# Kernel tuning notes

Hardware: AMD Instinct MI355X
Metric: run time of the kernel (lower is better)

Reference implementation:

```python
import jax, jax.numpy as jnp
import numpy as np

NBUS = 33
B33 = [(1,2),(2,3),(3,4),(4,5),(5,6),(6,7),(7,8),(8,9),(9,10),(10,11),(11,12),(12,13),(13,14),(14,15),(15,16),(16,17),(17,18),(2,19),(19,20),(20,21),(21,22),(3,23),(23,24),(24,25),(6,26),(26,27),(27,28),(28,29),(29,30),(30,31),(31,32),(32,33)]


def setup_inputs() -> dict:
    key = jax.random.key(0)
    k1, k2, k3 = jax.random.split(key, 3)
    B, W, M, F = 32, 128, 100, 8
    N, H, GH, K = NBUS, 256, 128, 3
    rng = np.random.default_rng(0)
    br = np.array(B33) - 1
    src = np.concatenate([br[:, 0], br[:, 1]])
    dst = np.concatenate([br[:, 1], br[:, 0]])
    w_half = rng.uniform(0.5, 2.0, size=br.shape[0]).astype(np.float32)
    p = lambda *s: jnp.asarray(rng.normal(0.0, 0.02, size=s).astype(np.float32))
    z = lambda *s: jnp.zeros(s, jnp.float32)
    return {
        'r_seq': jax.random.normal(k1, (B, W, M), jnp.float32),
        'feat_seq': jax.random.normal(k2, (B, W, F), jnp.float32),
        'x_wls_seq': jax.random.normal(k3, (B, W, 2 * N), jnp.float32),
        'edge_index': jnp.asarray(np.stack([src, dst]).astype(np.int32)),
        'edge_weight': jnp.asarray(np.concatenate([w_half, w_half])),
        'pre_w': p(F + 2, GH), 'pre_b': z(GH),
        'tag_w1': p(K + 1, GH, GH), 'tag_b1': z(GH),
        'tag_w2': p(K + 1, GH, GH), 'tag_b2': z(GH),
        'post_w': p(GH, H), 'post_b': z(H),
        'tp_w1': p(M + 2 * N, H), 'tp_b1': z(H),
        'tp_w2': p(H, H), 'tp_b2': z(H),
        'gru_wih0': p(H, 3 * H), 'gru_whh0': p(H, 3 * H), 'gru_bih0': z(3 * H), 'gru_bhh0': z(3 * H),
        'gru_wih1': p(H, 3 * H), 'gru_whh1': p(H, 3 * H), 'gru_bih1': z(3 * H), 'gru_bhh1': z(3 * H),
        'fg_w': p(H, H), 'fg_b': z(H),
        'fs_w': p(H, H), 'fs_b': z(H),
        'gate_w': p(2 * H, H), 'gate_b': z(H),
        'd1_w': p(H, H), 'd1_b': z(H),
        'd2_w': p(H, 2), 'd2_b': z(2),
    }


def _gru_layer(x, wih, whh, bih, bhh):
    # x: (B, W, Din); torch GRU gate order [r, z, n]
    def step(h, xt):
        gi = xt @ wih + bih
        gh = h @ whh + bhh
        ir, iz, inn = jnp.split(gi, 3, axis=-1)
        hr, hz, hn = jnp.split(gh, 3, axis=-1)
        r = jax.nn.sigmoid(ir + hr)
        zt = jax.nn.sigmoid(iz + hz)
        n = jnp.tanh(inn + r * hn)
        h = (1.0 - zt) * n + zt * h
        return h, h
    h0 = jnp.zeros((x.shape[0], whh.shape[0]), x.dtype)
    _, ys = jax.lax.scan(step, h0, jnp.swapaxes(x, 0, 1))
    return jnp.swapaxes(ys, 0, 1)


def _forward(r_seq, feat_seq, x_wls_seq, edge_index, edge_weight,
             pre_w, pre_b, tag_w1, tag_b1, tag_w2, tag_b2, post_w, post_b,
             tp_w1, tp_b1, tp_w2, tp_b2,
             gru_wih0, gru_whh0, gru_bih0, gru_bhh0,
             gru_wih1, gru_whh1, gru_bih1, gru_bhh1,
             fg_w, fg_b, fs_w, fs_b, gate_w, gate_b,
             d1_w, d1_b, d2_w, d2_b):
    B, W, M = r_seq.shape
    N = NBUS
    # ---- spatial branch (batched TAGConv, K=3, 2 layers) ----
    va = x_wls_seq[..., :N, None]
    vm = x_wls_seq[..., N:, None]
    x_nodes = jnp.concatenate([va, vm], axis=-1)                 # (B,W,N,2)
    feat_n = jnp.broadcast_to(feat_seq[:, :, None, :], (B, W, N, feat_seq.shape[-1]))
    gin = jnp.concatenate([feat_n, x_nodes], axis=-1) @ pre_w + pre_b  # (B,W,N,GH)
    g = gin.reshape(B * W, N, gin.shape[-1])
    src, dst = edge_index[0], edge_index[1]
    # gcn_norm (no self-loops), shared across all B*W graph copies
    deg = jnp.zeros((N,), g.dtype).at[dst].add(edge_weight)
    dinv = jnp.where(deg > 0, deg ** -0.5, 0.0)
    norm = dinv[src] * edge_weight * dinv[dst]                   # (E,)

    def prop(h):  # out[i] = sum_{j->i} norm * h[j], batched over graphs
        return jnp.zeros_like(h).at[:, dst].add(h[:, src] * norm[None, :, None])

    def tag(h, Wk, b):  # TAGConv: sum_k A^k h @ W_k + b
        out = h @ Wk[0]
        hk = h
        for k in range(1, Wk.shape[0]):
            hk = prop(hk)
            out = out + hk @ Wk[k]
        return out + b

    g = jax.nn.relu(tag(g, tag_w1, tag_b1))
    g = tag(g, tag_w2, tag_b2)
    g = g.reshape(B, W, N, -1) @ post_w + post_b                 # (B,W,N,H)
    # ---- temporal branch (MLP -> 2-layer GRU); E_time=None skips MHA ----
    s = jnp.concatenate([r_seq, x_wls_seq], axis=-1)
    s = jax.nn.relu(s @ tp_w1 + tp_b1)
    s = jax.nn.relu(s @ tp_w2 + tp_b2)
    s = _gru_layer(s, gru_wih0, gru_whh0, gru_bih0, gru_bhh0)
    s = _gru_layer(s, gru_wih1, gru_whh1, gru_bih1, gru_bhh1)    # (B,W,H)
    # ---- gated fusion + decoder ----
    g_t = g @ fg_w + fg_b                                        # (B,W,N,H)
    s_t = (s @ fs_w + fs_b)[:, :, None, :]                       # (B,W,1,H)
    s_full = jnp.broadcast_to(s_t, g_t.shape)
    alpha = jax.nn.sigmoid(jnp.concatenate([g_t, s_full], axis=-1) @ gate_w + gate_b)
    u = alpha * g_t + (1.0 - alpha) * s_full
    u = jax.nn.relu(u @ d1_w + d1_b) @ d2_w + d2_b               # (B,W,N,2)
    dx = jnp.concatenate([u[..., 0], u[..., 1]], axis=-1)        # (B,W,2N)
    return x_wls_seq + dx


def reference(r_seq, feat_seq, x_wls_seq, edge_index, edge_weight,
              pre_w, pre_b, tag_w1, tag_b1, tag_w2, tag_b2, post_w, post_b,
              tp_w1, tp_b1, tp_w2, tp_b2,
              gru_wih0, gru_whh0, gru_bih0, gru_bhh0,
              gru_wih1, gru_whh1, gru_bih1, gru_bhh1,
              fg_w, fg_b, fs_w, fs_b, gate_w, gate_b,
              d1_w, d1_b, d2_w, d2_b):
    return _forward(r_seq, feat_seq, x_wls_seq, edge_index, edge_weight,
                    pre_w, pre_b, tag_w1, tag_b1, tag_w2, tag_b2, post_w, post_b,
                    tp_w1, tp_b1, tp_w2, tp_b2,
                    gru_wih0, gru_whh0, gru_bih0, gru_bhh0,
                    gru_wih1, gru_whh1, gru_bih1, gru_bhh1,
                    fg_w, fg_b, fs_w, fs_b, gate_w, gate_b,
                    d1_w, d1_b, d2_w, d2_b)
```

## Files before the change

kernel.cpp:

```cpp
#include <hip/hip_runtime.h>
#include <hip/hip_fp16.h>
#include <cmath>

#define DEV __device__ __forceinline__

typedef unsigned short ushortT;
typedef short bs8 __attribute__((ext_vector_type(8)));
typedef float f32x4 __attribute__((ext_vector_type(4)));
typedef _Float16 f16x2 __attribute__((ext_vector_type(2)));

constexpr int kBW = 4096;
constexpr int kM = 100, kF = 8, kN = 33, kH = 256, kGH = 128, kE = 64;

constexpr int OFF_ROWPTR  = 0;
constexpr int OFF_COLSRC  = 64;
constexpr int OFF_COLNORM = 128;
constexpr int OFF_C       = 192;
constexpr int OFF_WC      = 512;
constexpr int OFF_SPRE    = 33280;
constexpr int OFF_GI      = OFF_SPRE + kBW * kH;
constexpr int OFF_SFUSE   = OFF_GI + kBW * 3 * kH;
constexpr int OFF_SGATE   = OFF_SFUSE + kBW * kH;
constexpr int OFF_WQ0     = OFF_SFUSE;
constexpr int OFF_WQ1     = OFF_SFUSE + 98304;
constexpr int WB_TW1  = 0;
constexpr int WB_TW2  = 65536;
constexpr int WB_WC   = 131072;
constexpr int WB_GATE = 163840;
constexpr int WB_D1   = 229376;
constexpr int WB_TOT  = 294912;

DEV float frcp(float x) { return __builtin_amdgcn_rcpf(x); }
DEV float fsig(float x) { return frcp(1.0f + __expf(-x)); }
DEV float ftanh(float x) { float e = __expf(2.0f * x); return 1.0f - 2.0f * frcp(e + 1.0f); }

DEV ushortT f2bf(float x) {
  unsigned u = __float_as_uint(x);
  unsigned r = u + 0x7fffu + ((u >> 16) & 1u);
  return (ushortT)(r >> 16);
}
DEV float bf2f(ushortT u) { return __uint_as_float(((unsigned)u) << 16); }

DEV f32x4 mfma16(bs8 a, bs8 b, f32x4 c) {
  return __builtin_amdgcn_mfma_f32_16x16x32_bf16(a, b, c, 0, 0, 0);
}
DEV bs8 ldb(const ushortT* p) { return *reinterpret_cast<const bs8*>(p); }

#if __has_builtin(__builtin_amdgcn_fdot2)
DEV float dot2(unsigned w, unsigned hp, float acc) {
  f16x2 wv = __builtin_bit_cast(f16x2, w);
  f16x2 hv = __builtin_bit_cast(f16x2, hp);
  return __builtin_amdgcn_fdot2(wv, hv, acc, false);
}
#else
DEV float dot2(unsigned w, unsigned hp, float acc) {
  f16x2 wv = __builtin_bit_cast(f16x2, w);
  f16x2 hv = __builtin_bit_cast(f16x2, hp);
  acc = fmaf((float)wv.x, (float)hv.x, acc);
  acc = fmaf((float)wv.y, (float)hv.y, acc);
  return acc;
}
#endif

__global__ void k_prep(const int* __restrict__ ei, const float* __restrict__ ew,
                       float* __restrict__ ws) {
  if (blockIdx.x != 0 || threadIdx.x != 0) return;
  int* rowptr = (int*)(ws + OFF_ROWPTR);
  int* colsrc = (int*)(ws + OFF_COLSRC);
  float* colnorm = ws + OFF_COLNORM;
  const int* src = ei;
  const int* dst = ei + kE;
  float deg[kN]; int cnt[kN];
  for (int n = 0; n < kN; ++n) { deg[n] = 0.f; cnt[n] = 0; }
  for (int e = 0; e < kE; ++e) { deg[dst[e]] += ew[e]; cnt[dst[e]]++; }
  float dinv[kN];
  for (int n = 0; n < kN; ++n) dinv[n] = deg[n] > 0.f ? 1.0f / sqrtf(deg[n]) : 0.f;
  int pos[kN];
  int run = 0;
  for (int n = 0; n < kN; ++n) { rowptr[n] = run; pos[n] = run; run += cnt[n]; }
  rowptr[kN] = run;
  for (int e = 0; e < kE; ++e) {
    int d = dst[e];
    int p = pos[d]++;
    colsrc[p] = src[e];
    colnorm[p] = dinv[src[e]] * ew[e] * dinv[d];
  }
}

__global__ void k_wcfold(const float* __restrict__ post_w, const float* __restrict__ post_b,
                         const float* __restrict__ fg_w, const float* __restrict__ fg_b,
                         float* __restrict__ ws) {
  const int j = threadIdx.x;
  if ((int)blockIdx.x < kGH) {
    const int k = blockIdx.x;
    float a = 0.f;
    #pragma unroll 4
    for (int m = 0; m < kH; ++m) a = fmaf(post_w[k * kH + m], fg_w[m * kH + j], a);
    ws[OFF_WC + k * kH + j] = a;
  } else {
    float a = fg_b[j];
    #pragma unroll 4
    for (int m = 0; m < kH; ++m) a = fmaf(post_b[m], fg_w[m * kH + j], a);
    ws[OFF_C + j] = a;
  }
}

__global__ void k_wq(const float* __restrict__ w0, const float* __restrict__ w1,
                     float* __restrict__ ws) {
  const int idx = blockIdx.x * 256 + threadIdx.x;
  if (idx >= 2 * 98304) return;
  const int layer = idx / 98304;
  const int rem = idx - layer * 98304;
  const int p = rem / 768, j = rem - p * 768;
  const float* w = layer ? w1 : w0;
  unsigned* dst = (unsigned*)(ws + (layer ? OFF_WQ1 : OFF_WQ0));
  __half2 v = __floats2half2_rn(w[(2 * p) * 768 + j], w[(2 * p + 1) * 768 + j]);
  dst[rem] = *reinterpret_cast<unsigned*>(&v);
}

__global__ void k_wprep(const float* __restrict__ tw1, const float* __restrict__ tw2,
                        const float* __restrict__ gatew, const float* __restrict__ d1w,
                        float* __restrict__ ws) {
  const int idx = blockIdx.x * 256 + threadIdx.x;
  if (idx >= WB_TOT) return;
  ushortT* WB = (ushortT*)(ws + OFF_GI);
  float v; int dst;
  if (idx < 65536) {
    int s = idx >> 14, r = idx & 16383, k = r >> 7, col = r & 127;
    v = tw1[(s << 14) + (k << 7) + col]; dst = WB_TW1 + (s << 14) + (col << 7) + k;
  } else if (idx < 131072) {
    int i = idx - 65536; int s = i >> 14, r = i & 16383, k = r >> 7, col = r & 127;
    v = tw2[(s << 14) + (k << 7) + col]; dst = WB_TW2 + (s << 14) + (col << 7) + k;
  } else if (idx < 163840) {
    int i = idx - 131072; int k = i & 127, col = i >> 7;
    v = ws[OFF_WC + (k << 8) + col]; dst = WB_WC + (col << 7) + k;
  } else if (idx < 229376) {
    int i = idx - 163840; int k = i & 255, col = i >> 8;
    v = gatew[(k << 8) + col]; dst = WB_GATE + (col << 8) + k;
  } else {
    int i = idx - 229376; int k = i & 255, col = i >> 8;
    v = d1w[(k << 8) + col]; dst = WB_D1 + (col << 8) + k;
  }
  WB[dst] = f2bf(v);
}

__global__ __launch_bounds__(256) void k_tpmlp(
    const float* __restrict__ r_seq, const float* __restrict__ x_wls,
    const float* __restrict__ w1, const float* __restrict__ b1,
    const float* __restrict__ w2, const float* __restrict__ b2,
    float* __restrict__ sout) {
  __shared__ float inr[16][kM + 2 * kN];
  __shared__ float h1[16][kH];
  const int bw0 = blockIdx.x * 16, tid = threadIdx.x;
  #pragma unroll
  for (int r = 0; r < 16; ++r) {
    for (int c = tid; c < kM + 2 * kN; c += 256)
      inr[r][c] = (c < kM) ? r_seq[(bw0 + r) * kM + c]
                           : x_wls[(bw0 + r) * 2 * kN + (c - kM)];
  }
  __syncthreads();
  float acc[16];
  {
    const float bb = b1[tid];
    #pragma unroll
    for (int r = 0; r < 16; ++r) acc[r] = bb;
  }
  for (int k = 0; k < kM + 2 * kN; ++k) {
    const float w = w1[k * kH + tid];
    #pragma unroll
    for (int r = 0; r < 16; ++r) acc[r] = fmaf(inr[r][k], w, acc[r]);
  }
  #pragma unroll
  for (int r = 0; r < 16; ++r) h1[r][tid] = fmaxf(acc[r], 0.f);
  __syncthreads();
  {
    const float bb = b2[tid];
    #pragma unroll
    for (int r = 0; r < 16; ++r) acc[r] = bb;
  }
  #pragma unroll 2
  for (int k = 0; k < kH; ++k) {
    const float w = w2[k * kH + tid];
    #pragma unroll
    for (int r = 0; r < 16; ++r) acc[r] = fmaf(h1[r][k], w, acc[r]);
  }
  #pragma unroll
  for (int r = 0; r < 16; ++r) sout[(bw0 + r) * kH + tid] = fmaxf(acc[r], 0.f);
}

__global__ __launch_bounds__(768) void k_gigemm(
    const float* __restrict__ sin, const float* __restrict__ wih,
    const float* __restrict__ bih, float* __restrict__ gi) {
  __shared__ float sr[16][kH];
  const int bw0 = blockIdx.x * 16, tid = threadIdx.x;
  for (int i = tid; i < 16 * kH; i += 768) sr[i >> 8][i & 255] = sin[bw0 * kH + i];
  __syncthreads();
  float acc[16];
  {
    const float bb = bih[tid];
    #pragma unroll
    for (int r = 0; r < 16; ++r) acc[r] = bb;
  }
  #pragma unroll 2
  for (int k = 0; k < kH; ++k) {
    const float w = wih[k * 768 + tid];
    #pragma unroll
    for (int r = 0; r < 16; ++r) acc[r] = fmaf(sr[r][k], w, acc[r]);
  }
  #pragma unroll
  for (int r = 0; r < 16; ++r) gi[(bw0 + r) * 768 + tid] = acc[r];
}

__global__ __launch_bounds__(768, 3) void k_scan(
    const float* __restrict__ gi, const float* __restrict__ wq,
    const float* __restrict__ bhh, float* __restrict__ sout) {
  __shared__ float h[kH];
  __shared__ __align__(16) unsigned hpk[kH / 2];
  __shared__ float gh[3 * kH];
  const int b = blockIdx.x, tid = threadIdx.x;
  const unsigned* wqp = (const unsigned*)wq;
  unsigned wr[128];
  #pragma unroll
  for (int p = 0; p < 128; ++p) wr[p] = wqp[p * 768 + tid];
  if (tid < kH) h[tid] = 0.f;
  if (tid < kH / 2) hpk[tid] = 0u;
  __syncthreads();
  const float bb = bhh[tid];
  for (int t = 0; t < 128; ++t) {
    const float* girow = gi + (b * 128 + t) * 768;
    float a0 = bb, a1 = 0.f, a2 = 0.f, a3 = 0.f;
    #pragma unroll
    for (int q = 0; q < 32; ++q) {
      const uint4 hp = *reinterpret_cast<const uint4*>(hpk + 4 * q);
      a0 = dot2(wr[4 * q + 0], hp.x, a0);
      a1 = dot2(wr[4 * q + 1], hp.y, a1);
      a2 = dot2(wr[4 * q + 2], hp.z, a2);
      a3 = dot2(wr[4 * q + 3], hp.w, a3);
    }
    gh[tid] = (a0 + a1) + (a2 + a3);
    __syncthreads();
    if (tid < kH) {
      float r = fsig(girow[tid] + gh[tid]);
      float z = fsig(girow[kH + tid] + gh[kH + tid]);
      float n = ftanh(fmaf(r, gh[2 * kH + tid], girow[2 * kH + tid]));
      float hn = (1.f - z) * n + z * h[tid];
      h[tid] = hn;
      reinterpret_cast<__half*>(hpk)[tid] = __float2half(hn);
      sout[(b * 128 + t) * kH + tid] = hn;
    }
    __syncthreads();
  }
}

__global__ __launch_bounds__(256) void k_fsgate(
    const float* __restrict__ s1, const float* __restrict__ fsw,
    const float* __restrict__ fsb, const float* __restrict__ gw,
    const float* __restrict__ gb, float* __restrict__ sfuse,
    float* __restrict__ sgate) {
  __shared__ float sr[16][kH], sf[16][kH];
  const int bw0 = blockIdx.x * 16, tid = threadIdx.x;
  for (int i = tid; i < 16 * kH; i += 256) sr[i >> 8][i & 255] = s1[bw0 * kH + i];
  __syncthreads();
  float acc[16];
  {
    const float bb = fsb[tid];
    #pragma unroll
    for (int r = 0; r < 16; ++r) acc[r] = bb;
  }
  #pragma unroll 2
  for (int k = 0; k < kH; ++k) {
    const float w = fsw[k * kH + tid];
    #pragma unroll
    for (int r = 0; r < 16; ++r) acc[r] = fmaf(sr[r][k], w, acc[r]);
  }
  #pragma unroll
  for (int r = 0; r < 16; ++r) { sf[r][tid] = acc[r]; sfuse[(bw0 + r) * kH + tid] = acc[r]; }
  __syncthreads();
  {
    const float bb = gb[tid];
    #pragma unroll
    for (int r = 0; r < 16; ++r) acc[r] = bb;
  }
  #pragma unroll 2
  for (int k = 0; k < kH; ++k) {
    const float w = gw[(kH + k) * kH + tid];
    #pragma unroll
    for (int r = 0; r < 16; ++r) acc[r] = fmaf(sf[r][k], w, acc[r]);
  }
  #pragma unroll
  for (int r = 0; r < 16; ++r) sgate[(bw0 + r) * kH + tid] = acc[r];
}


constexpr int SB0 = 0;
constexpr int SB1 = 36 * 136;
constexpr int S_TOT = 2 * 36 * 136;

DEV void propb(ushortT* __restrict__ dst, const ushortT* __restrict__ src,
               const int* __restrict__ rp, const int* __restrict__ cs,
               const float* __restrict__ cn) {
  for (int idx = threadIdx.x; idx < kN * 64; idx += 512) {
    const int n = idx >> 6, j2 = idx & 63;
    float a0 = 0.f, a1 = 0.f;
    const int p1 = rp[n + 1];
    for (int p = rp[n]; p < p1; ++p) {
      const unsigned v = *(const unsigned*)(src + cs[p] * 136 + 2 * j2);
      const float w = cn[p];
      a0 = fmaf(__uint_as_float(v << 16), w, a0);
      a1 = fmaf(__uint_as_float(v & 0xffff0000u), w, a1);
    }
    *(unsigned*)(dst + n * 136 + 2 * j2) = (unsigned)f2bf(a0) | ((unsigned)f2bf(a1) << 16);
  }
}

template <bool RELU>
DEV void tag_mfma(ushortT* __restrict__ Sb, const ushortT* __restrict__ WT,
                  const float* __restrict__ b, const int* __restrict__ rp,
                  const int* __restrict__ cs, const float* __restrict__ cn,
                  int wv, int lane) {
  const int lr = lane & 15, lg = lane >> 4;
  const int col = wv * 16 + lr;
  f32x4 acc[3];
  #pragma unroll
  for (int i = 0; i < 3; ++i) acc[i] = (f32x4){0.f, 0.f, 0.f, 0.f};
  #pragma unroll
  for (int s = 0; s < 4; ++s) {
    const ushortT* A = Sb + ((s & 1) ? SB1 : SB0);
    ushortT* Bn      = Sb + ((s & 1) ? SB0 : SB1);
    #pragma unroll
    for (int ks = 0; ks < 4; ++ks) {
      const int kof = ks * 32 + lg * 8;
      bs8 a0 = ldb(A + (lr) * 136 + kof);
      bs8 a1 = ldb(A + (16 + lr) * 136 + kof);
      bs8 a2 = ldb(A + (32 + lr) * 136 + kof);
      bs8 bb = ldb(WT + (s << 14) + (col << 7) + kof);
      acc[0] = mfma16(a0, bb, acc[0]);
      acc[1] = mfma16(a1, bb, acc[1]);
      acc[2] = mfma16(a2, bb, acc[2]);
    }
    if (s < 3) {
      propb(Bn, A, rp, cs, cn);
      __syncthreads();
    }
  }
  __syncthreads();
  const float bias = b[col];
  #pragma unroll
  for (int mt = 0; mt < 3; ++mt)
    #pragma unroll
    for (int r = 0; r < 4; ++r) {
      const int row = mt * 16 + lg * 4 + r;
      if (row < kN) {
        float x = acc[mt][r] + bias;
        if (RELU) x = fmaxf(x, 0.f);
        (Sb + SB0)[row * 136 + col] = f2bf(x);
      }
    }
  __syncthreads();
}

__global__ __launch_bounds__(512, 4) void k_fused(
    const float* __restrict__ feat_seq, const float* __restrict__ x_wls,
    const float* __restrict__ pre_w, const float* __restrict__ pre_b,
    const float* __restrict__ tb1, const float* __restrict__ tb2,
    const float* __restrict__ d1b, const float* __restrict__ d2w,
    const float* __restrict__ d2b, const float* __restrict__ ws,
    const float* __restrict__ sfuse, const float* __restrict__ sgate,
    float* __restrict__ out) {
  __shared__ __align__(16) ushortT S[S_TOT];
  __shared__ float sfrow[kH], sgrow[kH];
  __shared__ float xw[2 * kN];
  __shared__ float featl[kF];
  __shared__ int rp[kN + 1], cs[kE];
  __shared__ float cn[kE];
  __shared__ float part[8][48][2];
  const int tid = threadIdx.x, bw = blockIdx.x;
  const int wv = tid >> 6, lane = tid & 63;
  const int lr = lane & 15, lg = lane >> 4;
  const ushortT* WB = (const ushortT*)(ws + OFF_GI);
  ushortT* GT = S;

  if (tid < kH) sfrow[tid] = sfuse[bw * kH + tid];
  else if (tid < 2 * kH) sgrow[tid - kH] = sgate[bw * kH + (tid - kH)];
  if (tid < 2 * kN) xw[tid] = x_wls[bw * 2 * kN + tid];
  else if (tid >= 66 && tid < 66 + kF) featl[tid - 66] = feat_seq[bw * kF + (tid - 66)];
  if (tid >= 128 && tid < 128 + kN + 1) rp[tid - 128] = ((const int*)(ws + OFF_ROWPTR))[tid - 128];
  if (tid >= 192 && tid < 256) {
    cs[tid - 192] = ((const int*)(ws + OFF_COLSRC))[tid - 192];
    cn[tid - 192] = ws[OFF_COLNORM + (tid - 192)];
  }
  for (int i = tid; i < 3 * 136; i += 512) {
    S[SB0 + kN * 136 + i] = 0;
    S[SB1 + kN * 136 + i] = 0;
  }
  __syncthreads();

  for (int idx = tid; idx < kN * kGH; idx += 512) {
    const int n = idx >> 7, j = idx & 127;
    float a = pre_b[j];
    #pragma unroll
    for (int f = 0; f < kF; ++f) a = fmaf(featl[f], pre_w[f * kGH + j], a);
    a = fmaf(xw[n], pre_w[8 * kGH + j], a);
    a = fmaf(xw[kN + n], pre_w[9 * kGH + j], a);
    S[SB0 + n * 136 + j] = f2bf(a);
  }
  __syncthreads();

  tag_mfma<true >(S, WB + WB_TW1, tb1, rp, cs, cn, wv, lane);
  tag_mfma<false>(S, WB + WB_TW2, tb2, rp, cs, cn, wv, lane);

  {
    f32x4 acc[6];
    #pragma unroll
    for (int i = 0; i < 6; ++i) acc[i] = (f32x4){0.f, 0.f, 0.f, 0.f};
    #pragma unroll
    for (int ks = 0; ks < 4; ++ks) {
      const int kof = ks * 32 + lg * 8;
      bs8 a0 = ldb(S + SB0 + (lr) * 136 + kof);
      bs8 a1 = ldb(S + SB0 + (16 + lr) * 136 + kof);
      bs8 a2 = ldb(S + SB0 + (32 + lr) * 136 + kof);
      #pragma unroll
      for (int nt = 0; nt < 2; ++nt) {
        const int col = (wv * 2 + nt) * 16 + lr;
        bs8 bb = ldb(WB + WB_WC + (col << 7) + kof);
        acc[0 + nt] = mfma16(a0, bb, acc[0 + nt]);
        acc[2 + nt] = mfma16(a1, bb, acc[2 + nt]);
        acc[4 + nt] = mfma16(a2, bb, acc[4 + nt]);
      }
    }
    __syncthreads();
    #pragma unroll
    for (int mt = 0; mt < 3; ++mt)
      #pragma unroll
      for (int nt = 0; nt < 2; ++nt) {
        const int col = (wv * 2 + nt) * 16 + lr;
        const float cb = ws[OFF_C + col];
        const f32x4 v = acc[mt * 2 + nt];
        #pragma unroll
        for (int r = 0; r < 4; ++r) {
          const int row = mt * 16 + lg * 4 + r;
          if (row < kN) GT[row * 264 + col] = f2bf(v[r] + cb);
        }
      }
    __syncthreads();
  }

  {
    f32x4 acc[6];
    #pragma unroll
    for (int i = 0; i < 6; ++i) acc[i] = (f32x4){0.f, 0.f, 0.f, 0.f};
    #pragma unroll 2
    for (int ks = 0; ks < 8; ++ks) {
      const int kof = ks * 32 + lg * 8;
      const int r2 = (32 + lr) < 36 ? (32 + lr) : 35;
      bs8 a0 = ldb(GT + (lr) * 264 + kof);
      bs8 a1 = ldb(GT + (16 + lr) * 264 + kof);
      bs8 a2 = ldb(GT + r2 * 264 + kof);
      #pragma unroll
      for (int nt = 0; nt < 2; ++nt) {
        const int col = (wv * 2 + nt) * 16 + lr;
        bs8 bb = ldb(WB + WB_GATE + (col << 8) + kof);
        acc[0 + nt] = mfma16(a0, bb, acc[0 + nt]);
        acc[2 + nt] = mfma16(a1, bb, acc[2 + nt]);
        acc[4 + nt] = mfma16(a2, bb, acc[4 + nt]);
      }
    }
    #pragma unroll
    for (int mt = 0; mt < 3; ++mt)
      #pragma unroll
      for (int nt = 0; nt < 2; ++nt) {
        const int col = (wv * 2 + nt) * 16 + lr;
        const float sg = sgrow[col], sf = sfrow[col];
        #pragma unroll
        for (int r = 0; r < 4; ++r) {
          const int row = mt * 16 + lg * 4 + r;
          if (row < kN) {
            const float al = fsig(acc[mt * 2 + nt][r] + sg);
            const float gt = bf2f(GT[row * 264 + col]);
            acc[mt * 2 + nt][r] = al * gt + (1.f - al) * sf;
          }
        }
      }
    __syncthreads();
    #pragma unroll
    for (int mt = 0; mt < 3; ++mt)
      #pragma unroll
      for (int nt = 0; nt < 2; ++nt) {
        const int col = (wv * 2 + nt) * 16 + lr;
        #pragma unroll
        for (int r = 0; r < 4; ++r) {
          const int row = mt * 16 + lg * 4 + r;
          if (row < kN) GT[row * 264 + col] = f2bf(acc[mt * 2 + nt][r]);
        }
      }
    __syncthreads();
  }

  {
    f32x4 acc[6];
    #pragma unroll
    for (int i = 0; i < 6; ++i) acc[i] = (f32x4){0.f, 0.f, 0.f, 0.f};
    #pragma unroll 2
    for (int ks = 0; ks < 8; ++ks) {
      const int kof = ks * 32 + lg * 8;
      const int r2 = (32 + lr) < 36 ? (32 + lr) : 35;
      bs8 a0 = ldb(GT + (lr) * 264 + kof);
      bs8 a1 = ldb(GT + (16 + lr) * 264 + kof);
      bs8 a2 = ldb(GT + r2 * 264 + kof);
      #pragma unroll
      for (int nt = 0; nt < 2; ++nt) {
        const int col = (wv * 2 + nt) * 16 + lr;
        bs8 bb = ldb(WB + WB_D1 + (col << 8) + kof);
        acc[0 + nt] = mfma16(a0, bb, acc[0 + nt]);
        acc[2 + nt] = mfma16(a1, bb, acc[2 + nt]);
        acc[4 + nt] = mfma16(a2, bb, acc[4 + nt]);
      }
    }
    float p0[3][4], p1[3][4];
    #pragma unroll
    for (int mt = 0; mt < 3; ++mt)
      #pragma unroll
      for (int r = 0; r < 4; ++r) { p0[mt][r] = 0.f; p1[mt][r] = 0.f; }
    #pragma unroll
    for (int nt = 0; nt < 2; ++nt) {
      const int col = (wv * 2 + nt) * 16 + lr;
      const float db = d1b[col];
      const float2 dp = *reinterpret_cast<const float2*>(d2w + col * 2);
      #pragma unroll
      for (int mt = 0; mt < 3; ++mt)
        #pragma unroll
        for (int r = 0; r < 4; ++r) {
          const float v = fmaxf(acc[mt * 2 + nt][r] + db, 0.f);
          p0[mt][r] = fmaf(v, dp.x, p0[mt][r]);
          p1[mt][r] = fmaf(v, dp.y, p1[mt][r]);
        }
    }
    #pragma unroll
    for (int mt = 0; mt < 3; ++mt)
      #pragma unroll
      for (int r = 0; r < 4; ++r) {
        #pragma unroll
        for (int off = 1; off < 16; off <<= 1) {
          p0[mt][r] += __shfl_xor(p0[mt][r], off, 64);
          p1[mt][r] += __shfl_xor(p1[mt][r], off, 64);
        }
      }
    if (lr == 0) {
      #pragma unroll
      for (int mt = 0; mt < 3; ++mt)
        #pragma unroll
        for (int r = 0; r < 4; ++r) {
          const int row = mt * 16 + lg * 4 + r;
          part[wv][row][0] = p0[mt][r];
          part[wv][row][1] = p1[mt][r];
        }
    }
    __syncthreads();
    if (tid < 66) {
      const int c = tid >= 33 ? 1 : 0;
      const int n = tid - 33 * c;
      float s = d2b[c];
      #pragma unroll
      for (int w = 0; w < 8; ++w) s += part[w][n][c];
      out[bw * 66 + tid] = xw[tid] + s;
    }
  }
}

extern "C" void kernel_launch(void* const* d_in, const int* in_sizes, int n_in,
                              void* d_out, int out_size, void* d_ws, size_t ws_size,
                              hipStream_t stream) {
  const float* r_seq  = (const float*)d_in[0];
  const float* feat   = (const float*)d_in[1];
  const float* x_wls  = (const float*)d_in[2];
  const int*   eidx   = (const int*)d_in[3];
  const float* ew     = (const float*)d_in[4];
  const float* pre_w  = (const float*)d_in[5];
  const float* pre_b  = (const float*)d_in[6];
  const float* tag_w1 = (const float*)d_in[7];
  const float* tag_b1 = (const float*)d_in[8];
  const float* tag_w2 = (const float*)d_in[9];
  const float* tag_b2 = (const float*)d_in[10];
  const float* post_w = (const float*)d_in[11];
  const float* post_b = (const float*)d_in[12];
  const float* tp_w1  = (const float*)d_in[13];
  const float* tp_b1  = (const float*)d_in[14];
  const float* tp_w2  = (const float*)d_in[15];
  const float* tp_b2  = (const float*)d_in[16];
  const float* wih0   = (const float*)d_in[17];
  const float* whh0   = (const float*)d_in[18];
  const float* bih0   = (const float*)d_in[19];
  const float* bhh0   = (const float*)d_in[20];
  const float* wih1   = (const float*)d_in[21];
  const float* whh1   = (const float*)d_in[22];
  const float* bih1   = (const float*)d_in[23];
  const float* bhh1   = (const float*)d_in[24];
  const float* fg_w   = (const float*)d_in[25];
  const float* fg_b   = (const float*)d_in[26];
  const float* fs_w   = (const float*)d_in[27];
  const float* fs_b   = (const float*)d_in[28];
  const float* gate_w = (const float*)d_in[29];
  const float* gate_b = (const float*)d_in[30];
  const float* d1_w   = (const float*)d_in[31];
  const float* d1_b   = (const float*)d_in[32];
  const float* d2_w   = (const float*)d_in[33];
  const float* d2_b   = (const float*)d_in[34];
  float* ws = (float*)d_ws;
  float* outp = (float*)d_out;

  k_prep<<<1, 64, 0, stream>>>(eidx, ew, ws);
  k_wcfold<<<kGH + 1, kH, 0, stream>>>(post_w, post_b, fg_w, fg_b, ws);
  k_wq<<<768, 256, 0, stream>>>(whh0, whh1, ws);
  k_tpmlp<<<kBW / 16, 256, 0, stream>>>(r_seq, x_wls, tp_w1, tp_b1, tp_w2, tp_b2,
                                        ws + OFF_SPRE);
  k_gigemm<<<kBW / 16, 768, 0, stream>>>(ws + OFF_SPRE, wih0, bih0, ws + OFF_GI);
  k_scan<<<32, 768, 0, stream>>>(ws + OFF_GI, ws + OFF_WQ0, bhh0, ws + OFF_SPRE);
  k_gigemm<<<kBW / 16, 768, 0, stream>>>(ws + OFF_SPRE, wih1, bih1, ws + OFF_GI);
  k_scan<<<32, 768, 0, stream>>>(ws + OFF_GI, ws + OFF_WQ1, bhh1, ws + OFF_SPRE);
  k_wprep<<<(WB_TOT + 255) / 256, 256, 0, stream>>>(tag_w1, tag_w2, gate_w, d1_w, ws);
  k_fsgate<<<kBW / 16, 256, 0, stream>>>(ws + OFF_SPRE, fs_w, fs_b, gate_w, gate_b,
                                         ws + OFF_SFUSE, ws + OFF_SGATE);
  k_fused<<<kBW, 512, 0, stream>>>(feat, x_wls, pre_w, pre_b, tag_b1, tag_b2,
                                   d1_b, d2_w, d2_b, ws, ws + OFF_SFUSE,
                                   ws + OFF_SGATE, outp);
}
```

Before: 1.030 ms.

## Restructure GRU scan to one thread per hidden unit with double-buffered state

Rewrites the recurrent GRU scan so each of 256 threads computes all three gate rows for its hidden unit, holding 384 packed fp16 weight registers, instead of 768 threads each computing one gate row. This removes the shared gh exchange and one of the two block barriers per timestep, and double-buffers the packed hidden state so a single barrier suffices. The cost is heavy register pressure, 384 weight registers plus accumulators, which risks spilling, and fewer waves per block to hide latency on the serial path.

```diff
diff --git a/kernel.cpp b/kernel.cpp
--- a/kernel.cpp
+++ b/kernel.cpp
@@ -211,43 +211,51 @@
   for (int r = 0; r < 16; ++r) gi[(bw0 + r) * 768 + tid] = acc[r];
 }
 
-__global__ __launch_bounds__(768, 3) void k_scan(
+__global__ __launch_bounds__(256, 1) void k_scan(
     const float* __restrict__ gi, const float* __restrict__ wq,
     const float* __restrict__ bhh, float* __restrict__ sout) {
-  __shared__ float h[kH];
-  __shared__ __align__(16) unsigned hpk[kH / 2];
-  __shared__ float gh[3 * kH];
-  const int b = blockIdx.x, tid = threadIdx.x;
+  __shared__ __align__(16) unsigned hpk[2][kH / 2];
+  const int b = blockIdx.x, j = threadIdx.x;
   const unsigned* wqp = (const unsigned*)wq;
-  unsigned wr[128];
-  #pragma unroll
-  for (int p = 0; p < 128; ++p) wr[p] = wqp[p * 768 + tid];
-  if (tid < kH) h[tid] = 0.f;
-  if (tid < kH / 2) hpk[tid] = 0u;
-  __syncthreads();
-  const float bb = bhh[tid];
+  unsigned wA[128], wB[128], wC[128];
+  #pragma unroll 8
+  for (int p = 0; p < 128; ++p) {
+    wA[p] = wqp[p * 768 + j];
+    wB[p] = wqp[p * 768 + 256 + j];
+    wC[p] = wqp[p * 768 + 512 + j];
+  }
+  const float bR = bhh[j], bZ = bhh[kH + j], bN = bhh[2 * kH + j];
+  if (j < kH / 2) hpk[0][j] = 0u;
+  float h = 0.f;
+  __syncthreads();
+  const float* gbase = gi + b * 128 * 768 + j;
   for (int t = 0; t < 128; ++t) {
-    const float* girow = gi + (b * 128 + t) * 768;
-    float a0 = bb, a1 = 0.f, a2 = 0.f, a3 = 0.f;
+    const float* g = gbase + t * 768;
+    const float gA = g[0], gB = g[256], gC = g[512];
+    float aR0 = bR, aR1 = 0.f, aZ0 = bZ, aZ1 = 0.f, aN0 = bN, aN1 = 0.f;
+    const unsigned* hb = hpk[t & 1];
     #pragma unroll
     for (int q = 0; q < 32; ++q) {
-      const uint4 hp = *reinterpret_cast<const uint4*>(hpk + 4 * q);
-      a0 = dot2(wr[4 * q + 0], hp.x, a0);
-      a1 = dot2(wr[4 * q + 1], hp.y, a1);
-      a2 = dot2(wr[4 * q + 2], hp.z, a2);
-      a3 = dot2(wr[4 * q + 3], hp.w, a3);
-    }
-    gh[tid] = (a0 + a1) + (a2 + a3);
-    __syncthreads();
-    if (tid < kH) {
-      float r = fsig(girow[tid] + gh[tid]);
-      float z = fsig(girow[kH + tid] + gh[kH + tid]);
-      float n = ftanh(fmaf(r, gh[2 * kH + tid], girow[2 * kH + tid]));
-      float hn = (1.f - z) * n + z * h[tid];
-      h[tid] = hn;
-      reinterpret_cast<__half*>(hpk)[tid] = __float2half(hn);
-      sout[(b * 128 + t) * kH + tid] = hn;
-    }
+      const uint4 hp = *reinterpret_cast<const uint4*>(hb + 4 * q);
+      aR0 = dot2(wA[4 * q + 0], hp.x, aR0);
+      aZ0 = dot2(wB[4 * q + 0], hp.x, aZ0);
+      aN0 = dot2(wC[4 * q + 0], hp.x, aN0);
+      aR1 = dot2(wA[4 * q + 1], hp.y, aR1);
+      aZ1 = dot2(wB[4 * q + 1], hp.y, aZ1);
+      aN1 = dot2(wC[4 * q + 1], hp.y, aN1);
+      aR0 = dot2(wA[4 * q + 2], hp.z, aR0);
+      aZ0 = dot2(wB[4 * q + 2], hp.z, aZ0);
+      aN0 = dot2(wC[4 * q + 2], hp.z, aN0);
+      aR1 = dot2(wA[4 * q + 3], hp.w, aR1);
+      aZ1 = dot2(wB[4 * q + 3], hp.w, aZ1);
+      aN1 = dot2(wC[4 * q + 3], hp.w, aN1);
+    }
+    const float r = fsig(gA + aR0 + aR1);
+    const float z = fsig(gB + aZ0 + aZ1);
+    const float n = ftanh(fmaf(r, aN0 + aN1, gC));
+    h = (1.f - z) * n + z * h;
+    reinterpret_cast<__half*>(hpk[(t + 1) & 1])[j] = __float2half(h);
+    sout[(b * 128 + t) * kH + j] = h;
     __syncthreads();
   }
 }
@@ -614,9 +622,9 @@
   k_tpmlp<<<kBW / 16, 256, 0, stream>>>(r_seq, x_wls, tp_w1, tp_b1, tp_w2, tp_b2,
                                         ws + OFF_SPRE);
   k_gigemm<<<kBW / 16, 768, 0, stream>>>(ws + OFF_SPRE, wih0, bih0, ws + OFF_GI);
-  k_scan<<<32, 768, 0, stream>>>(ws + OFF_GI, ws + OFF_WQ0, bhh0, ws + OFF_SPRE);
+  k_scan<<<32, 256, 0, stream>>>(ws + OFF_GI, ws + OFF_WQ0, bhh0, ws + OFF_SPRE);
   k_gigemm<<<kBW / 16, 768, 0, stream>>>(ws + OFF_SPRE, wih1, bih1, ws + OFF_GI);
-  k_scan<<<32, 768, 0, stream>>>(ws + OFF_GI, ws + OFF_WQ1, bhh1, ws + OFF_SPRE);
+  k_scan<<<32, 256, 0, stream>>>(ws + OFF_GI, ws + OFF_WQ1, bhh1, ws + OFF_SPRE);
   k_wprep<<<(WB_TOT + 255) / 256, 256, 0, stream>>>(tag_w1, tag_w2, gate_w, d1_w, ws);
   k_fsgate<<<kBW / 16, 256, 0, stream>>>(ws + OFF_SPRE, fs_w, fs_b, gate_w, gate_b,
                                          ws + OFF_SFUSE, ws + OFF_SGATE);
```

Result: slower. 3.455 ms (+235.4%).
